# Performance work log

Measured on AMD Instinct MI355X. Metric: run time of the kernel, lower is better.

The kernel has to match this reference:

```python
import jax, jax.numpy as jnp
import numpy as np

DIM = 2048
N_HEADS = 16
HEAD_DIM = DIM // N_HEADS  # 128
B, S = 2, 2048


def setup_inputs() -> dict:
    key = jax.random.key(0)
    ks = jax.random.split(key, 12)
    sc = 1.0 / np.sqrt(DIM)
    inp = {
        "x": jax.random.normal(ks[0], (B, S, DIM), jnp.float32),
        # freqs for rotary: angle theta per (position, pair)
        "freqs_cos": jnp.cos(jnp.outer(jnp.arange(S, dtype=jnp.float32),
                                        1.0 / (10000.0 ** (jnp.arange(0, HEAD_DIM, 2, dtype=jnp.float32) / HEAD_DIM)))),
        "freqs_sin": jnp.sin(jnp.outer(jnp.arange(S, dtype=jnp.float32),
                                        1.0 / (10000.0 ** (jnp.arange(0, HEAD_DIM, 2, dtype=jnp.float32) / HEAD_DIM)))),
        "wq_w": jax.random.normal(ks[1], (DIM, DIM), jnp.float32) * sc,
        "wq_b": jax.random.normal(ks[2], (DIM,), jnp.float32) * sc,
        "wk_w": jax.random.normal(ks[3], (DIM, DIM), jnp.float32) * sc,
        "wk_b": jax.random.normal(ks[4], (DIM,), jnp.float32) * sc,
        "wv_w": jax.random.normal(ks[5], (DIM, DIM), jnp.float32) * sc,
        "wv_b": jax.random.normal(ks[6], (DIM,), jnp.float32) * sc,
        "wo_w": jax.random.normal(ks[7], (DIM, DIM), jnp.float32) * sc,
        "wo_b": jax.random.normal(ks[8], (DIM,), jnp.float32) * sc,
    }
    return inp


def _rope(xq, xk, cos, sin):
    # xq/xk: [B, S, H, D]; cos/sin: [S, D//2]
    def rot(t):
        tr = t.reshape(*t.shape[:-1], -1, 2)  # [B,S,H,D//2,2]
        t0, t1 = tr[..., 0], tr[..., 1]
        c = cos[None, :, None, :]
        s = sin[None, :, None, :]
        o0 = t0 * c - t1 * s
        o1 = t0 * s + t1 * c
        return jnp.stack([o0, o1], axis=-1).reshape(t.shape)
    return rot(xq), rot(xk)


def reference(x, freqs_cos, freqs_sin, wq_w, wq_b, wk_w, wk_b, wv_w, wv_b, wo_w, wo_b):
    b, s, _ = x.shape
    xq = (x @ wq_w.T + wq_b).reshape(b, s, N_HEADS, HEAD_DIM)
    xk = (x @ wk_w.T + wk_b).reshape(b, s, N_HEADS, HEAD_DIM)
    xv = (x @ wv_w.T + wv_b).reshape(b, s, N_HEADS, HEAD_DIM)
    xq, xk = _rope(xq, xk, freqs_cos, freqs_sin)
    # NOTE: original has NO softmax — raw scaled scores are used directly.
    scores = jnp.einsum('bqhd,bkhd->bhqk', xq, xk) / jnp.sqrt(jnp.float32(HEAD_DIM))
    out = jnp.einsum('bhqk,bkhd->bqhd', scores, xv).reshape(b, s, DIM)
    return out @ wo_w.T + wo_b
```

## Files before the change

### kernel.cpp

```cpp
#include <hip/hip_runtime.h>
#include <hip/hip_bf16.h>

#define DIMN 2048
#define NQKV 6144
#define NH 16
#define HD 128
#define BSZ 2
#define SEQ 2048
#define ROWS (BSZ*SEQ)

typedef short short8 __attribute__((ext_vector_type(8)));
typedef float f32x4 __attribute__((ext_vector_type(4)));

__device__ __forceinline__ unsigned short f2bf(float f) {
    __hip_bfloat16 h = __float2bfloat16(f);
    unsigned short u; __builtin_memcpy(&u, &h, 2); return u;
}

__device__ __forceinline__ void gld_lds16(const void* g, void* l) {
    __builtin_amdgcn_global_load_lds(
        (const __attribute__((address_space(1))) void*)g,
        (__attribute__((address_space(3))) void*)l, 16, 0, 0);
}

__global__ void cvt_all(const float* __restrict__ x, const float* __restrict__ wq,
                        const float* __restrict__ wk, const float* __restrict__ wv,
                        const float* __restrict__ wo,
                        unsigned short* __restrict__ Xb, unsigned short* __restrict__ Wcat,
                        unsigned short* __restrict__ Wo2) {
    int bid = blockIdx.x;
    const float* in; unsigned short* out; int base;
    if      (bid <  8192) { in = x;  out = Xb;             base = bid; }
    else if (bid < 12288) { in = wq; out = Wcat;           base = bid - 8192; }
    else if (bid < 16384) { in = wk; out = Wcat + 4194304; base = bid - 12288; }
    else if (bid < 20480) { in = wv; out = Wcat + 8388608; base = bid - 16384; }
    else                  { in = wo; out = Wo2;            base = bid - 20480; }
    int i = (base * 256 + threadIdx.x) * 4;
    float4 v = *(const float4*)(in + i);
    ushort4 o; o.x = f2bf(v.x); o.y = f2bf(v.y); o.z = f2bf(v.z); o.w = f2bf(v.w);
    *(ushort4*)(out + i) = o;
}


template<int MODE>
__global__ __launch_bounds__(512, 2) void gemm256(
    const unsigned short* __restrict__ A, int lda,
    const unsigned short* __restrict__ B, int ldb,
    const float* __restrict__ b0, const float* __restrict__ b1, const float* __restrict__ b2,
    const float* __restrict__ fcos, const float* __restrict__ fsin,
    void* __restrict__ C, int ldc, int K)
{
    __shared__ __align__(16) unsigned short As[32768];
    __shared__ __align__(16) unsigned short Bs[32768];

    const int t  = threadIdx.x;
    const int l  = t & 63;
    const int w  = t >> 6;
    const int wr = w >> 2;
    const int wc = w & 3;
    const int fr = l & 15, fq = l >> 4;

    const int xcd = blockIdx.x & 7;
    const int j   = blockIdx.x >> 3;
    int mt, nt;
    if (MODE == 0) {
        if (j < 32) { mt = (xcd & 1) * 8 + (j >> 2); nt = (xcd >> 1) * 4 + (j & 3); }
        else { const int p = j - 32, c = xcd >> 1;
               mt = (c & 1) * 8 + (xcd & 1) * 4 + (p >> 2); nt = (4 + (c >> 1)) * 4 + (p & 3); }
    } else {
        mt = (xcd >> 1) * 4 + (j >> 2);
        nt = (xcd & 1) * 4 + (j & 3);
    }
    const int m0 = mt * 256;
    const int n0 = nt * 256;

    const unsigned short* Bsel = B;
    if (MODE == 1 && m0 >= 2048) Bsel += (size_t)2048 * 2048;

    const int srow = t >> 3;
    const int scol = ((t & 7) ^ (srow & 7)) * 8;
    const unsigned short* aS = A    + (size_t)(m0 + srow) * lda + scol;
    const unsigned short* bS = Bsel + (size_t)(n0 + srow) * ldb + scol;

#define STG_A(KT, H) do { \
    const unsigned short* s_ = aS + (size_t)(H) * 128 * lda + (size_t)(KT) * 64; \
    gld_lds16(s_,                    &As[(((KT) & 1) << 14) + ((H) << 13) + t * 8]); \
    gld_lds16(s_ + (size_t)64 * lda, &As[(((KT) & 1) << 14) + ((H) << 13) + 4096 + t * 8]); \
  } while (0)
#define STG_B(KT, H) do { \
    const unsigned short* s_ = bS + (size_t)(H) * 128 * ldb + (size_t)(KT) * 64; \
    gld_lds16(s_,                    &Bs[(((KT) & 1) << 14) + ((H) << 13) + t * 8]); \
    gld_lds16(s_ + (size_t)64 * ldb, &Bs[(((KT) & 1) << 14) + ((H) << 13) + 4096 + t * 8]); \
  } while (0)

    const int cK0 = (fq ^ (fr & 7)) * 8;
    const int cK1 = ((4 + fq) ^ (fr & 7)) * 8;
    const int aB0 = wr * 8192 + fr * 64;
    const int bB0 = wc * 4096 + fr * 64;

    const unsigned aA0 = (unsigned)(size_t)&As[aB0 + cK0];
    const unsigned aA1 = (unsigned)(size_t)&As[aB0 + cK1];
    const unsigned bA0 = (unsigned)(size_t)&Bs[bB0 + cK0];
    const unsigned bA1 = (unsigned)(size_t)&Bs[bB0 + cK1];

    short8 aF[4][2], bF0[2][2], bF1[2][2];
    f32x4  acc[8][4] = {};

#define DSR(dst, areg, OFF) \
    asm volatile("ds_read_b128 %0, %1 offset:%2" : "=v"(dst) : "v"(areg), "n"(OFF))

#define RD_A(DDB, QM) do { \
    DSR(aF[0][0], aA0, (DDB) + (QM) * 8192 + 0);    DSR(aF[0][1], aA1, (DDB) + (QM) * 8192 + 0); \
    DSR(aF[1][0], aA0, (DDB) + (QM) * 8192 + 2048); DSR(aF[1][1], aA1, (DDB) + (QM) * 8192 + 2048); \
    DSR(aF[2][0], aA0, (DDB) + (QM) * 8192 + 4096); DSR(aF[2][1], aA1, (DDB) + (QM) * 8192 + 4096); \
    DSR(aF[3][0], aA0, (DDB) + (QM) * 8192 + 6144); DSR(aF[3][1], aA1, (DDB) + (QM) * 8192 + 6144); \
  } while (0)
#define RD_B(DDB, QN, BF) do { \
    DSR(BF[0][0], bA0, (DDB) + (QN) * 4096 + 0);    DSR(BF[0][1], bA1, (DDB) + (QN) * 4096 + 0); \
    DSR(BF[1][0], bA0, (DDB) + (QN) * 4096 + 2048); DSR(BF[1][1], bA1, (DDB) + (QN) * 4096 + 2048); \
  } while (0)

#define BAR() asm volatile("s_barrier" ::: "memory")

#define MM(QM, QN, BF) do { \
    _Pragma("unroll") for (int m2 = 0; m2 < 4; ++m2) \
      _Pragma("unroll") for (int n2 = 0; n2 < 2; ++n2) { \
        acc[(QM)*4+m2][(QN)*2+n2] = __builtin_amdgcn_mfma_f32_16x16x32_bf16( \
            aF[m2][0], BF[n2][0], acc[(QM)*4+m2][(QN)*2+n2], 0, 0, 0); \
        acc[(QM)*4+m2][(QN)*2+n2] = __builtin_amdgcn_mfma_f32_16x16x32_bf16( \
            aF[m2][1], BF[n2][1], acc[(QM)*4+m2][(QN)*2+n2], 0, 0, 0); } \
  } while (0)

#define TILE(KT, DDB) do { \
    if ((KT) + 1 < ktT) { \
        STG_A((KT) + 1, 0); STG_A((KT) + 1, 1); \
        STG_B((KT) + 1, 0); STG_B((KT) + 1, 1); \
    } \
    RD_A(DDB, 0); RD_B(DDB, 0, bF0); RD_B(DDB, 1, bF1); \
    asm volatile("s_waitcnt lgkmcnt(4)"); \
    __builtin_amdgcn_sched_barrier(0); \
    __builtin_amdgcn_s_setprio(1); \
    MM(0, 0, bF0); \
    asm volatile("s_waitcnt lgkmcnt(0)"); \
    __builtin_amdgcn_sched_barrier(0); \
    MM(0, 1, bF1); \
    __builtin_amdgcn_s_setprio(0); \
    RD_A(DDB, 1); \
    asm volatile("s_waitcnt lgkmcnt(0)"); \
    __builtin_amdgcn_sched_barrier(0); \
    __builtin_amdgcn_s_setprio(1); \
    MM(1, 0, bF0); MM(1, 1, bF1); \
    __builtin_amdgcn_s_setprio(0); \
    asm volatile("s_waitcnt vmcnt(0)"); \
    __builtin_amdgcn_sched_barrier(0); \
    BAR(); \
  } while (0)

    const int ktT = K >> 6;

    STG_A(0, 0); STG_A(0, 1);
    STG_B(0, 0); STG_B(0, 1);
    asm volatile("s_waitcnt vmcnt(0)");
    __builtin_amdgcn_sched_barrier(0);
    BAR();

    for (int kt = 0; kt < ktT; kt += 2) {
        TILE(kt, 0);
        TILE(kt + 1, 32768);
    }

#undef TILE
#undef MM
#undef BAR
#undef RD_A
#undef RD_B
#undef DSR
#undef STG_A
#undef STG_B

    #pragma unroll
    for (int mi = 0; mi < 8; ++mi) {
        #pragma unroll
        for (int ni = 0; ni < 4; ++ni) {
            #pragma unroll
            for (int j2 = 0; j2 < 4; ++j2) {
                const int r  = m0 + wr * 128 + mi * 16 + fq * 4 + j2;
                const int cg = n0 + wc * 64 + ni * 16 + fr;
                float v = acc[mi][ni][j2];
                if (MODE == 0) {
                    v += (cg < 2048) ? b0[cg] : ((cg < 4096) ? b1[cg - 2048] : b2[cg - 4096]);
                    if (cg < 4096) {
                        const int s = r & (SEQ - 1);
                        const int i = (cg >> 1) & 63;
                        const float cs = fcos[s * 64 + i];
                        const float sn = fsin[s * 64 + i];
                        const float p  = __shfl_xor(v, 1);
                        v = (fr & 1) ? (p * sn + v * cs) : (v * cs - p * sn);
                    }
                    ((unsigned short*)C)[(size_t)r * ldc + cg] = f2bf(v);
                } else {
                    v += b0[cg];
                    ((float*)C)[(size_t)r * ldc + cg] = v;
                }
            }
        }
    }
}

template<int OUT_BF16, int HAS_BIAS>
__device__ __forceinline__ void gemm_tile_core(
    const unsigned short* __restrict__ A, int lda,
    const unsigned short* __restrict__ B, int ldb,
    const float* __restrict__ bias,
    void* __restrict__ Cptr, int ldc, int K)
{
    __shared__ __align__(16) unsigned short As[128 * 64];
    __shared__ __align__(16) unsigned short Bs[128 * 64];

    const int t  = threadIdx.x;
    const int l  = t & 63;
    const int w  = t >> 6;
    const int wr = w >> 1, wc = w & 1;
    const int fr = l & 15, fq = l >> 4;

    f32x4 acc[4][4] = {};

    const int srow = t >> 3;
    const int scol = (t & 7) * 8;

    for (int k0 = 0; k0 < K; k0 += 64) {
        __syncthreads();
        #pragma unroll
        for (int r = 0; r < 4; ++r) {
            gld_lds16(A + (size_t)(r * 32 + srow) * lda + k0 + scol, &As[(r * 32 + srow) * 64 + scol]);
            gld_lds16(B + (size_t)(r * 32 + srow) * ldb + k0 + scol, &Bs[(r * 32 + srow) * 64 + scol]);
        }
        __syncthreads();
        #pragma unroll
        for (int kk = 0; kk < 2; ++kk) {
            short8 a[4], b[4];
            #pragma unroll
            for (int mi = 0; mi < 4; ++mi)
                a[mi] = *(const short8*)&As[(wr * 64 + mi * 16 + fr) * 64 + kk * 32 + fq * 8];
            #pragma unroll
            for (int ni = 0; ni < 4; ++ni)
                b[ni] = *(const short8*)&Bs[(wc * 64 + ni * 16 + fr) * 64 + kk * 32 + fq * 8];
            #pragma unroll
            for (int mi = 0; mi < 4; ++mi)
                #pragma unroll
                for (int ni = 0; ni < 4; ++ni)
                    acc[mi][ni] = __builtin_amdgcn_mfma_f32_16x16x32_bf16(a[mi], b[ni], acc[mi][ni], 0, 0, 0);
        }
    }

    #pragma unroll
    for (int mi = 0; mi < 4; ++mi) {
        #pragma unroll
        for (int ni = 0; ni < 4; ++ni) {
            #pragma unroll
            for (int j = 0; j < 4; ++j) {
                int rr = wr * 64 + mi * 16 + fq * 4 + j;
                int cc = wc * 64 + ni * 16 + fr;
                float v = acc[mi][ni][j];
                if (HAS_BIAS) v += bias[cc];
                if (OUT_BF16) ((unsigned short*)Cptr)[(size_t)rr * ldc + cc] = f2bf(v);
                else          ((float*)Cptr)[(size_t)rr * ldc + cc] = v;
            }
        }
    }
}

__global__ __launch_bounds__(256) void ktv_kernel(
    const unsigned short* __restrict__ QKV, float* __restrict__ part)
{
    const int ks = blockIdx.x;
    const int bh = blockIdx.y;
    const int b = bh >> 4, h = bh & 15;
    const unsigned short* Kbase = QKV + (size_t)(b * SEQ + ks * 256) * NQKV + 2048 + h * HD;
    const unsigned short* Vbase = QKV + (size_t)(b * SEQ + ks * 256) * NQKV + 4096 + h * HD;

    __shared__ __align__(16) unsigned short Ks_[64 * 128];
    __shared__ __align__(16) unsigned short Vs_[64 * 128];

    const int t  = threadIdx.x;
    const int l  = t & 63;
    const int w  = t >> 6;
    const int wr = w >> 1, wc = w & 1;
    const int fr = l & 15, fq = l >> 4;

    f32x4 acc[4][4] = {};

    const int srow = t >> 4;
    const int scol = (t & 15) * 8;

    for (int sc = 0; sc < 4; ++sc) {
        __syncthreads();
        #pragma unroll
        for (int r = 0; r < 4; ++r) {
            gld_lds16(Kbase + (size_t)(sc * 64 + r * 16 + srow) * NQKV + scol, &Ks_[(r * 16 + srow) * 128 + scol]);
            gld_lds16(Vbase + (size_t)(sc * 64 + r * 16 + srow) * NQKV + scol, &Vs_[(r * 16 + srow) * 128 + scol]);
        }
        __syncthreads();
        #pragma unroll
        for (int kk = 0; kk < 2; ++kk) {
            short8 a[4], bb[4];
            #pragma unroll
            for (int mi = 0; mi < 4; ++mi)
                #pragma unroll
                for (int i = 0; i < 8; ++i)
                    a[mi][i] = (short)Ks_[(kk * 32 + fq * 8 + i) * 128 + wr * 64 + mi * 16 + fr];
            #pragma unroll
            for (int ni = 0; ni < 4; ++ni)
                #pragma unroll
                for (int i = 0; i < 8; ++i)
                    bb[ni][i] = (short)Vs_[(kk * 32 + fq * 8 + i) * 128 + wc * 64 + ni * 16 + fr];
            #pragma unroll
            for (int mi = 0; mi < 4; ++mi)
                #pragma unroll
                for (int ni = 0; ni < 4; ++ni)
                    acc[mi][ni] = __builtin_amdgcn_mfma_f32_16x16x32_bf16(a[mi], bb[ni], acc[mi][ni], 0, 0, 0);
        }
    }

    float* base = part + ((size_t)bh * 8 + ks) * 16384;
    #pragma unroll
    for (int mi = 0; mi < 4; ++mi)
        #pragma unroll
        for (int ni = 0; ni < 4; ++ni)
            #pragma unroll
            for (int j = 0; j < 4; ++j)
                base[(wr * 64 + mi * 16 + fq * 4 + j) * 128 + wc * 64 + ni * 16 + fr] = acc[mi][ni][j];
}

__global__ void ktv_reduce(const float* __restrict__ part, unsigned short* __restrict__ M2t) {
    int idx = blockIdx.x * 256 + threadIdx.x;
    int bh = idx >> 14, rem = idx & 16383;
    const float* p = part + ((size_t)bh * 8) * 16384 + rem;
    float s = 0.f;
    #pragma unroll
    for (int k = 0; k < 8; ++k) s += p[(size_t)k * 16384];
    M2t[idx] = f2bf(s * 0.08838834764831845f);
}

__global__ __launch_bounds__(256) void w2_gemm(
    const unsigned short* __restrict__ Wo2, const unsigned short* __restrict__ M2t,
    unsigned short* __restrict__ W2)
{
    const int mt = blockIdx.x;
    const int bh = blockIdx.y;
    const int b = bh >> 4, h = bh & 15;
    const unsigned short* A = Wo2 + (size_t)(mt * 128) * DIMN + h * HD;
    const unsigned short* B = M2t + (size_t)bh * HD * HD;
    unsigned short* Cp = W2 + (size_t)b * DIMN * DIMN + (size_t)(mt * 128) * DIMN + h * HD;
    gemm_tile_core<1, 0>(A, DIMN, B, HD, nullptr, Cp, DIMN, HD);
}

extern "C" void kernel_launch(void* const* d_in, const int* in_sizes, int n_in,
                              void* d_out, int out_size, void* d_ws, size_t ws_size,
                              hipStream_t stream) {
    const float* x    = (const float*)d_in[0];
    const float* fcos = (const float*)d_in[1];
    const float* fsin = (const float*)d_in[2];
    const float* wq   = (const float*)d_in[3];
    const float* bq   = (const float*)d_in[4];
    const float* wk   = (const float*)d_in[5];
    const float* bk   = (const float*)d_in[6];
    const float* wv   = (const float*)d_in[7];
    const float* bv   = (const float*)d_in[8];
    const float* wo   = (const float*)d_in[9];
    const float* bo   = (const float*)d_in[10];
    float* out = (float*)d_out;

    char* ws = (char*)d_ws;
    size_t off = 0;
    auto alloc = [&](size_t bytes) { char* p = ws + off; off += (bytes + 255) & ~(size_t)255; return p; };

    unsigned short* Xb   = (unsigned short*)alloc((size_t)ROWS * DIMN * 2);
    unsigned short* Wcat = (unsigned short*)alloc((size_t)NQKV * DIMN * 2);
    unsigned short* Wo2  = (unsigned short*)alloc((size_t)DIMN * DIMN * 2);
    unsigned short* QKV  = (unsigned short*)alloc((size_t)ROWS * NQKV * 2);
    float*          part = (float*)alloc((size_t)32 * 8 * HD * HD * 4);
    unsigned short* M2t  = (unsigned short*)alloc((size_t)32 * HD * HD * 2);
    unsigned short* W2   = (unsigned short*)alloc((size_t)BSZ * DIMN * DIMN * 2);

    cvt_all<<<24576, 256, 0, stream>>>(x, wq, wk, wv, wo, Xb, Wcat, Wo2);

    gemm256<0><<<384, 512, 0, stream>>>(
        Xb, DIMN, Wcat, DIMN, bq, bk, bv, fcos, fsin, QKV, NQKV, DIMN);

    ktv_kernel<<<dim3(8, 32), 256, 0, stream>>>(QKV, part);
    ktv_reduce<<<(32 * 16384) / 256, 256, 0, stream>>>(part, M2t);

    w2_gemm<<<dim3(16, 32), 256, 0, stream>>>(Wo2, M2t, W2);

    gemm256<1><<<128, 512, 0, stream>>>(
        QKV, NQKV, W2, DIMN, bo, nullptr, nullptr, nullptr, nullptr, out, DIMN, DIMN);
}
```

Measured before the change: 228.8 us.

## Replace 256x256 pipelined GEMM with simple 128x128 single-buffered GEMM

Swaps the hand-scheduled 256x256-tile, double-buffered, 8-wave GEMM (inline ds_reads, setprio, sched barriers) for a plain 128x128 tile, 4-wave kernel with a single LDS buffer and __syncthreads around each k-step. Grids grow to 1536 and 512 blocks, giving more blocks per GEMM and better CU fill for the smaller output GEMM. The cost is lower data reuse per tile, no overlap of global loads with MFMA work, and the loss of the tuned instruction schedule.

```diff
diff --git a/kernel.cpp b/kernel.cpp
--- a/kernel.cpp
+++ b/kernel.cpp
@@ -43,148 +43,74 @@
 
 
 template<int MODE>
-__global__ __launch_bounds__(512, 2) void gemm256(
+__global__ __launch_bounds__(256) void gemm97(
     const unsigned short* __restrict__ A, int lda,
     const unsigned short* __restrict__ B, int ldb,
     const float* __restrict__ b0, const float* __restrict__ b1, const float* __restrict__ b2,
     const float* __restrict__ fcos, const float* __restrict__ fsin,
     void* __restrict__ C, int ldc, int K)
 {
-    __shared__ __align__(16) unsigned short As[32768];
-    __shared__ __align__(16) unsigned short Bs[32768];
+    __shared__ __align__(16) unsigned short As[128 * 64];
+    __shared__ __align__(16) unsigned short Bs[128 * 64];
 
     const int t  = threadIdx.x;
     const int l  = t & 63;
     const int w  = t >> 6;
-    const int wr = w >> 2;
-    const int wc = w & 3;
+    const int wr = w >> 1, wc = w & 1;
     const int fr = l & 15, fq = l >> 4;
 
     const int xcd = blockIdx.x & 7;
     const int j   = blockIdx.x >> 3;
     int mt, nt;
-    if (MODE == 0) {
-        if (j < 32) { mt = (xcd & 1) * 8 + (j >> 2); nt = (xcd >> 1) * 4 + (j & 3); }
-        else { const int p = j - 32, c = xcd >> 1;
-               mt = (c & 1) * 8 + (xcd & 1) * 4 + (p >> 2); nt = (4 + (c >> 1)) * 4 + (p & 3); }
-    } else {
-        mt = (xcd >> 1) * 4 + (j >> 2);
-        nt = (xcd & 1) * 4 + (j & 3);
-    }
-    const int m0 = mt * 256;
-    const int n0 = nt * 256;
+    if (MODE == 0) { nt = xcd * 6 + j % 6; mt = j / 6; }
+    else           { nt = xcd * 2 + (j & 1); mt = j >> 1; }
+    const int m0 = mt * 128;
+    const int n0 = nt * 128;
 
     const unsigned short* Bsel = B;
     if (MODE == 1 && m0 >= 2048) Bsel += (size_t)2048 * 2048;
 
     const int srow = t >> 3;
-    const int scol = ((t & 7) ^ (srow & 7)) * 8;
+    const int sc   = t & 7;
+    const int scol = (sc ^ (srow & 7)) * 8;
     const unsigned short* aS = A    + (size_t)(m0 + srow) * lda + scol;
     const unsigned short* bS = Bsel + (size_t)(n0 + srow) * ldb + scol;
 
-#define STG_A(KT, H) do { \
-    const unsigned short* s_ = aS + (size_t)(H) * 128 * lda + (size_t)(KT) * 64; \
-    gld_lds16(s_,                    &As[(((KT) & 1) << 14) + ((H) << 13) + t * 8]); \
-    gld_lds16(s_ + (size_t)64 * lda, &As[(((KT) & 1) << 14) + ((H) << 13) + 4096 + t * 8]); \
-  } while (0)
-#define STG_B(KT, H) do { \
-    const unsigned short* s_ = bS + (size_t)(H) * 128 * ldb + (size_t)(KT) * 64; \
-    gld_lds16(s_,                    &Bs[(((KT) & 1) << 14) + ((H) << 13) + t * 8]); \
-    gld_lds16(s_ + (size_t)64 * ldb, &Bs[(((KT) & 1) << 14) + ((H) << 13) + 4096 + t * 8]); \
-  } while (0)
-
-    const int cK0 = (fq ^ (fr & 7)) * 8;
-    const int cK1 = ((4 + fq) ^ (fr & 7)) * 8;
-    const int aB0 = wr * 8192 + fr * 64;
-    const int bB0 = wc * 4096 + fr * 64;
-
-    const unsigned aA0 = (unsigned)(size_t)&As[aB0 + cK0];
-    const unsigned aA1 = (unsigned)(size_t)&As[aB0 + cK1];
-    const unsigned bA0 = (unsigned)(size_t)&Bs[bB0 + cK0];
-    const unsigned bA1 = (unsigned)(size_t)&Bs[bB0 + cK1];
-
-    short8 aF[4][2], bF0[2][2], bF1[2][2];
-    f32x4  acc[8][4] = {};
-
-#define DSR(dst, areg, OFF) \
-    asm volatile("ds_read_b128 %0, %1 offset:%2" : "=v"(dst) : "v"(areg), "n"(OFF))
-
-#define RD_A(DDB, QM) do { \
-    DSR(aF[0][0], aA0, (DDB) + (QM) * 8192 + 0);    DSR(aF[0][1], aA1, (DDB) + (QM) * 8192 + 0); \
-    DSR(aF[1][0], aA0, (DDB) + (QM) * 8192 + 2048); DSR(aF[1][1], aA1, (DDB) + (QM) * 8192 + 2048); \
-    DSR(aF[2][0], aA0, (DDB) + (QM) * 8192 + 4096); DSR(aF[2][1], aA1, (DDB) + (QM) * 8192 + 4096); \
-    DSR(aF[3][0], aA0, (DDB) + (QM) * 8192 + 6144); DSR(aF[3][1], aA1, (DDB) + (QM) * 8192 + 6144); \
-  } while (0)
-#define RD_B(DDB, QN, BF) do { \
-    DSR(BF[0][0], bA0, (DDB) + (QN) * 4096 + 0);    DSR(BF[0][1], bA1, (DDB) + (QN) * 4096 + 0); \
-    DSR(BF[1][0], bA0, (DDB) + (QN) * 4096 + 2048); DSR(BF[1][1], bA1, (DDB) + (QN) * 4096 + 2048); \
-  } while (0)
-
-#define BAR() asm volatile("s_barrier" ::: "memory")
-
-#define MM(QM, QN, BF) do { \
-    _Pragma("unroll") for (int m2 = 0; m2 < 4; ++m2) \
-      _Pragma("unroll") for (int n2 = 0; n2 < 2; ++n2) { \
-        acc[(QM)*4+m2][(QN)*2+n2] = __builtin_amdgcn_mfma_f32_16x16x32_bf16( \
-            aF[m2][0], BF[n2][0], acc[(QM)*4+m2][(QN)*2+n2], 0, 0, 0); \
-        acc[(QM)*4+m2][(QN)*2+n2] = __builtin_amdgcn_mfma_f32_16x16x32_bf16( \
-            aF[m2][1], BF[n2][1], acc[(QM)*4+m2][(QN)*2+n2], 0, 0, 0); } \
-  } while (0)
-
-#define TILE(KT, DDB) do { \
-    if ((KT) + 1 < ktT) { \
-        STG_A((KT) + 1, 0); STG_A((KT) + 1, 1); \
-        STG_B((KT) + 1, 0); STG_B((KT) + 1, 1); \
-    } \
-    RD_A(DDB, 0); RD_B(DDB, 0, bF0); RD_B(DDB, 1, bF1); \
-    asm volatile("s_waitcnt lgkmcnt(4)"); \
-    __builtin_amdgcn_sched_barrier(0); \
-    __builtin_amdgcn_s_setprio(1); \
-    MM(0, 0, bF0); \
-    asm volatile("s_waitcnt lgkmcnt(0)"); \
-    __builtin_amdgcn_sched_barrier(0); \
-    MM(0, 1, bF1); \
-    __builtin_amdgcn_s_setprio(0); \
-    RD_A(DDB, 1); \
-    asm volatile("s_waitcnt lgkmcnt(0)"); \
-    __builtin_amdgcn_sched_barrier(0); \
-    __builtin_amdgcn_s_setprio(1); \
-    MM(1, 0, bF0); MM(1, 1, bF1); \
-    __builtin_amdgcn_s_setprio(0); \
-    asm volatile("s_waitcnt vmcnt(0)"); \
-    __builtin_amdgcn_sched_barrier(0); \
-    BAR(); \
-  } while (0)
-
-    const int ktT = K >> 6;
-
-    STG_A(0, 0); STG_A(0, 1);
-    STG_B(0, 0); STG_B(0, 1);
-    asm volatile("s_waitcnt vmcnt(0)");
-    __builtin_amdgcn_sched_barrier(0);
-    BAR();
-
-    for (int kt = 0; kt < ktT; kt += 2) {
-        TILE(kt, 0);
-        TILE(kt + 1, 32768);
-    }
-
-#undef TILE
-#undef MM
-#undef BAR
-#undef RD_A
-#undef RD_B
-#undef DSR
-#undef STG_A
-#undef STG_B
+    f32x4 acc[4][4] = {};
+
+    for (int k0 = 0; k0 < K; k0 += 64) {
+        __syncthreads();
+        #pragma unroll
+        for (int r = 0; r < 4; ++r) {
+            gld_lds16(aS + (size_t)(r * 32) * lda + k0, &As[r * 2048 + t * 8]);
+            gld_lds16(bS + (size_t)(r * 32) * ldb + k0, &Bs[r * 2048 + t * 8]);
+        }
+        __syncthreads();
+        #pragma unroll
+        for (int kk = 0; kk < 2; ++kk) {
+            const int co = (((kk << 2) | fq) ^ (fr & 7)) * 8;
+            short8 a[4], b[4];
+            #pragma unroll
+            for (int mi = 0; mi < 4; ++mi)
+                a[mi] = *(const short8*)&As[(wr * 64 + mi * 16 + fr) * 64 + co];
+            #pragma unroll
+            for (int ni = 0; ni < 4; ++ni)
+                b[ni] = *(const short8*)&Bs[(wc * 64 + ni * 16 + fr) * 64 + co];
+            #pragma unroll
+            for (int mi = 0; mi < 4; ++mi)
+                #pragma unroll
+                for (int ni = 0; ni < 4; ++ni)
+                    acc[mi][ni] = __builtin_amdgcn_mfma_f32_16x16x32_bf16(a[mi], b[ni], acc[mi][ni], 0, 0, 0);
+        }
+    }
 
     #pragma unroll
-    for (int mi = 0; mi < 8; ++mi) {
+    for (int mi = 0; mi < 4; ++mi) {
         #pragma unroll
         for (int ni = 0; ni < 4; ++ni) {
             #pragma unroll
             for (int j2 = 0; j2 < 4; ++j2) {
-                const int r  = m0 + wr * 128 + mi * 16 + fq * 4 + j2;
+                const int r  = m0 + wr * 64 + mi * 16 + fq * 4 + j2;
                 const int cg = n0 + wc * 64 + ni * 16 + fr;
                 float v = acc[mi][ni][j2];
                 if (MODE == 0) {
@@ -385,7 +311,7 @@
 
     cvt_all<<<24576, 256, 0, stream>>>(x, wq, wk, wv, wo, Xb, Wcat, Wo2);
 
-    gemm256<0><<<384, 512, 0, stream>>>(
+    gemm97<0><<<1536, 256, 0, stream>>>(
         Xb, DIMN, Wcat, DIMN, bq, bk, bv, fcos, fsin, QKV, NQKV, DIMN);
 
     ktv_kernel<<<dim3(8, 32), 256, 0, stream>>>(QKV, part);
@@ -393,6 +319,6 @@
 
     w2_gemm<<<dim3(16, 32), 256, 0, stream>>>(Wo2, M2t, W2);
 
-    gemm256<1><<<128, 512, 0, stream>>>(
+    gemm97<1><<<512, 256, 0, stream>>>(
         QKV, NQKV, W2, DIMN, bo, nullptr, nullptr, nullptr, nullptr, out, DIMN, DIMN);
 }
```

After: 234.6 us. 1.03x slower.
